# Kernel optimization log

Measured on AMD Instinct MI355X. Metric: run time of the kernel, lower is better.

## Reference

```python
import jax, jax.numpy as jnp
import numpy as np

EMB = 64
HEADS = 8
POOL = 2          # instruction_pool_size
TOK = 10          # tokens_per_instruction
CAP = 32          # max_capped_distances per axis -> tables have 2*CAP-1 rows


def setup_inputs() -> dict:
    key = jax.random.key(0)
    ks = jax.random.split(key, 8)
    scale = float(np.sqrt(6.0 / (TOK + EMB)))  # xavier-ish; exact init irrelevant for math
    return {
        "enc_cross": jax.random.uniform(ks[0], (POOL, TOK, EMB), jnp.float32, -scale, scale),
        "enc_h": jax.random.uniform(ks[1], (2 * CAP - 1, EMB), jnp.float32, -scale, scale),
        "enc_w": jax.random.uniform(ks[2], (2 * CAP - 1, EMB), jnp.float32, -scale, scale),
        "enc_d": jax.random.uniform(ks[3], (2 * CAP - 1, EMB), jnp.float32, -scale, scale),
        "w_cross": jax.random.uniform(ks[4], (HEADS, EMB), jnp.float32, -scale, scale),
        "w_h": jax.random.uniform(ks[5], (HEADS, EMB), jnp.float32, -scale, scale),
        "w_w": jax.random.uniform(ks[6], (HEADS, EMB), jnp.float32, -scale, scale),
        "w_d": jax.random.uniform(ks[7], (HEADS, EMB), jnp.float32, -scale, scale),
        "dim_q": 4116,
        "dim_k": 4116,
        "dim_i": 20,
        "dim_h": 16,
        "dim_w": 16,
        "dim_d": 16,
    }


def _rel_embed(n, table):
    # table: [2*cap-1, emb]; returns gathered relative-position embeddings [n, n, emb]
    cap = (table.shape[0] + 1) // 2
    r = jnp.arange(n)
    idx = jnp.clip(r[None, :] - r[:, None] + cap - 1, 0, 2 * cap - 2)
    return table[idx]


def reference(enc_cross, enc_h, enc_w, enc_d, w_cross, w_h, w_w, w_d,
              dim_q, dim_k, dim_i, dim_h, dim_w, dim_d):
    tok = enc_cross.shape[1]
    emb = enc_cross.shape[-1]
    heads = w_cross.shape[0]
    inv_temperature = emb ** -0.5

    # instruction -> content embeddings: first n_cat tables concatenated (label_indices=None path)
    n_cat = dim_i // tok
    cross_emb = enc_cross[:n_cat].reshape(1, n_cat * tok, emb)  # [1, dim_i, emb]

    row_e = _rel_embed(dim_h, enc_h)  # [h, h, emb]
    col_e = _rel_embed(dim_w, enc_w)  # [w, w, emb]
    dep_e = _rel_embed(dim_d, enc_d)  # [d, d, emb]

    cross_s = jnp.einsum('hc,bnc->bhn', w_cross, cross_emb)        # [1, heads, dim_i]
    row_s = jnp.einsum('hc,nmc->hnm', w_h, row_e)[None]            # [1, heads, h, h]
    col_s = jnp.einsum('hc,nmc->hnm', w_w, col_e)[None]            # [1, heads, w, w]
    dep_s = jnp.einsum('hc,nmc->hnm', w_d, dep_e)[None]            # [1, heads, d, d]

    # broadcast-add over (i j k | l m n) -> [1, heads, h, w, d, h, w, d]
    content = (row_s[:, :, :, None, None, :, None, None]
               + col_s[:, :, None, :, None, None, :, None]
               + dep_s[:, :, None, None, :, None, None, :]) / 3.0
    S = dim_h * dim_w * dim_d
    content = content.reshape(1, heads, S, S)

    scores = jnp.zeros((1, heads, dim_q, dim_k), jnp.float32)
    # instruction bias block: rows dim_i:, cols :dim_i
    scores = scores.at[:, :, dim_i:, :dim_i].set(
        jnp.broadcast_to(cross_s[:, :, None, :], (1, heads, dim_q - dim_i, dim_i)))
    # content bias block: rows dim_i:, cols dim_i:
    scores = scores.at[:, :, dim_i:, dim_i:].set(content)
    return scores * inv_temperature
```

## Files before the change

kernel.cpp:

```cpp
#include <hip/hip_runtime.h>


#define EMB 64
#define NHEADS 8
#define DIM_I 20
#define DIM_Q 4116
#define NCHUNK 1029

__global__ __launch_bounds__(256) void tables_kernel(
    const float* __restrict__ enc_cross,
    const float* __restrict__ enc_h,
    const float* __restrict__ enc_w,
    const float* __restrict__ enc_d,
    const float* __restrict__ w_cross,
    const float* __restrict__ w_h,
    const float* __restrict__ w_w,
    const float* __restrict__ w_d,
    float* __restrict__ tabs)
{
    const int tid = blockIdx.x * blockDim.x + threadIdx.x;
    const int total = NHEADS * DIM_I + 3 * NHEADS * 256;
    if (tid >= total) return;

    if (tid < NHEADS * DIM_I) {
        const int h = tid / DIM_I;
        const int n = tid % DIM_I;
        const float* wv = w_cross + h * EMB;
        const float* ev = enc_cross + n * EMB;
        float acc = 0.f;
        #pragma unroll
        for (int c = 0; c < EMB; ++c) acc += wv[c] * ev[c];
        tabs[tid] = acc * 0.125f;
    } else {
        const int u = tid - NHEADS * DIM_I;
        const int table = u >> 11;
        const int v = u & 2047;
        const int h = v >> 8;
        const int i = (v >> 4) & 15;
        const int l = v & 15;
        const int ridx = l - i + 31;
        const float* wv;
        const float* ev;
        if (table == 0)      { wv = w_h + h * EMB; ev = enc_h + ridx * EMB; }
        else if (table == 1) { wv = w_w + h * EMB; ev = enc_w + ridx * EMB; }
        else                 { wv = w_d + h * EMB; ev = enc_d + ridx * EMB; }
        float acc = 0.f;
        #pragma unroll
        for (int c = 0; c < EMB; ++c) acc += wv[c] * ev[c];
        tabs[tid] = acc * (0.125f / 3.0f);
    }
}

__global__ __launch_bounds__(256) void fill_kernel(
    const float* __restrict__ tabs, float* __restrict__ out)
{
    const int q = blockIdx.x;
    const int h = blockIdx.y;

    float4* rowp = (float4*)(out + ((size_t)h * DIM_Q + q) * DIM_Q);

    if (q < DIM_I) {
        const float4 z = make_float4(0.f, 0.f, 0.f, 0.f);
        for (int t = threadIdx.x; t < NCHUNK; t += 256) rowp[t] = z;
        return;
    }

    const float* cross  = tabs + h * DIM_I;
    const float* row_s  = tabs + 160 + h * 256;
    const float* col_s  = tabs + 160 + 2048 + h * 256;
    const float* dep_s  = tabs + 160 + 4096 + h * 256;

    const int r  = q - DIM_I;
    const int i  = r >> 8;
    const int j  = (r >> 4) & 15;
    const int kk = r & 15;
    const float* rs_row = row_s + i * 16;
    const float* cs_row = col_s + j * 16;
    const float* ds_row = dep_s + kk * 16;

    for (int t = threadIdx.x; t < NCHUNK; t += 256) {
        float4 v;
        if (t < 5) {
            const int k0 = 4 * t;
            v.x = cross[k0 + 0];
            v.y = cross[k0 + 1];
            v.z = cross[k0 + 2];
            v.w = cross[k0 + 3];
        } else {
            const int c0 = 4 * t - DIM_I;
            const int l  = c0 >> 8;
            const int m  = (c0 >> 4) & 15;
            const int n0 = c0 & 15;
            const float base = rs_row[l] + cs_row[m];
            v.x = base + ds_row[n0 + 0];
            v.y = base + ds_row[n0 + 1];
            v.z = base + ds_row[n0 + 2];
            v.w = base + ds_row[n0 + 3];
        }
        rowp[t] = v;
    }
}

extern "C" void kernel_launch(void* const* d_in, const int* in_sizes, int n_in,
                              void* d_out, int out_size, void* d_ws, size_t ws_size,
                              hipStream_t stream)
{
    const float* enc_cross = (const float*)d_in[0];
    const float* enc_h     = (const float*)d_in[1];
    const float* enc_w     = (const float*)d_in[2];
    const float* enc_d     = (const float*)d_in[3];
    const float* w_cross   = (const float*)d_in[4];
    const float* w_h       = (const float*)d_in[5];
    const float* w_w       = (const float*)d_in[6];
    const float* w_d       = (const float*)d_in[7];

    float* tabs = (float*)d_ws;

    tables_kernel<<<dim3(25), dim3(256), 0, stream>>>(
        enc_cross, enc_h, enc_w, enc_d, w_cross, w_h, w_w, w_d, tabs);

    fill_kernel<<<dim3(DIM_Q, NHEADS), dim3(256), 0, stream>>>(
        tabs, (float*)d_out);
}
```

Baseline: 567.1 us.

## Restructure fill with LDS-staged tables, nontemporal stores, wave-parallel table dots

The table kernel now computes each 64-element dot product with one wave and a shuffle reduction, which launches far more threads. The fill kernel now has each block write 16 consecutive rows for a fixed (i,j) pair. It stages the row+col base sums and the depth table in LDS and writes with nontemporal vector stores. The 20 zero rows are split across two dedicated blocks per head. The aim is to cut per-element global table reads and cache pollution in this write-bound ~540 MB output, at the cost of fewer, larger blocks (2064 total) and a serial kk loop per block.

New measurement: 611.1 us. 1.08x slower.

```diff
diff --git a/kernel.cpp b/kernel.cpp
--- a/kernel.cpp
+++ b/kernel.cpp
@@ -6,6 +6,12 @@
 #define DIM_I 20
 #define DIM_Q 4116
 #define NCHUNK 1029
+#define OFF_ROW 160
+#define OFF_COL (160 + 2048)
+#define OFF_DEP (160 + 4096)
+#define N_DOTS 6304
+
+typedef float v4f __attribute__((ext_vector_type(4)));
 
 __global__ __launch_bounds__(256) void tables_kernel(
     const float* __restrict__ enc_cross,
@@ -18,86 +24,91 @@
     const float* __restrict__ w_d,
     float* __restrict__ tabs)
 {
-    const int tid = blockIdx.x * blockDim.x + threadIdx.x;
-    const int total = NHEADS * DIM_I + 3 * NHEADS * 256;
-    if (tid >= total) return;
+    const int wid  = (blockIdx.x * 256 + threadIdx.x) >> 6;
+    const int lane = threadIdx.x & 63;
+    if (wid >= N_DOTS) return;
 
-    if (tid < NHEADS * DIM_I) {
-        const int h = tid / DIM_I;
-        const int n = tid % DIM_I;
-        const float* wv = w_cross + h * EMB;
-        const float* ev = enc_cross + n * EMB;
-        float acc = 0.f;
-        #pragma unroll
-        for (int c = 0; c < EMB; ++c) acc += wv[c] * ev[c];
-        tabs[tid] = acc * 0.125f;
+    const float* wv;
+    const float* ev;
+    float scale;
+    int outidx;
+    if (wid < 160) {
+        const int h = wid / DIM_I;
+        const int n = wid % DIM_I;
+        wv = w_cross + h * EMB;
+        ev = enc_cross + n * EMB;
+        scale = 0.125f;
+        outidx = wid;
     } else {
-        const int u = tid - NHEADS * DIM_I;
+        const int u = wid - 160;
         const int table = u >> 11;
         const int v = u & 2047;
         const int h = v >> 8;
         const int i = (v >> 4) & 15;
         const int l = v & 15;
         const int ridx = l - i + 31;
-        const float* wv;
-        const float* ev;
         if (table == 0)      { wv = w_h + h * EMB; ev = enc_h + ridx * EMB; }
         else if (table == 1) { wv = w_w + h * EMB; ev = enc_w + ridx * EMB; }
         else                 { wv = w_d + h * EMB; ev = enc_d + ridx * EMB; }
-        float acc = 0.f;
-        #pragma unroll
-        for (int c = 0; c < EMB; ++c) acc += wv[c] * ev[c];
-        tabs[tid] = acc * (0.125f / 3.0f);
+        scale = 0.125f / 3.0f;
+        outidx = 160 + u;
     }
+
+    float p = wv[lane] * ev[lane];
+    #pragma unroll
+    for (int off = 32; off >= 1; off >>= 1)
+        p += __shfl_xor(p, off, 64);
+    if (lane == 0) tabs[outidx] = p * scale;
 }
 
 __global__ __launch_bounds__(256) void fill_kernel(
     const float* __restrict__ tabs, float* __restrict__ out)
 {
-    const int q = blockIdx.x;
-    const int h = blockIdx.y;
+    const int h   = blockIdx.y;
+    const int r   = blockIdx.x;
+    const int tid = threadIdx.x;
+    float* outh = out + (size_t)h * DIM_Q * DIM_Q;
 
-    float4* rowp = (float4*)(out + ((size_t)h * DIM_Q + q) * DIM_Q);
-
-    if (q < DIM_I) {
-        const float4 z = make_float4(0.f, 0.f, 0.f, 0.f);
-        for (int t = threadIdx.x; t < NCHUNK; t += 256) rowp[t] = z;
+    if (r >= 256) {
+        v4f* p = (v4f*)outh + (size_t)(r - 256) * 10290;
+        const v4f z = {0.f, 0.f, 0.f, 0.f};
+        for (int t = tid; t < 10290; t += 256)
+            __builtin_nontemporal_store(z, p + t);
         return;
     }
 
-    const float* cross  = tabs + h * DIM_I;
-    const float* row_s  = tabs + 160 + h * 256;
-    const float* col_s  = tabs + 160 + 2048 + h * 256;
-    const float* dep_s  = tabs + 160 + 4096 + h * 256;
+    __shared__ __align__(16) float Base[256];
+    __shared__ __align__(16) float dep[256];
+    __shared__ float cross20[DIM_I];
 
-    const int r  = q - DIM_I;
-    const int i  = r >> 8;
-    const int j  = (r >> 4) & 15;
-    const int kk = r & 15;
-    const float* rs_row = row_s + i * 16;
-    const float* cs_row = col_s + j * 16;
-    const float* ds_row = dep_s + kk * 16;
+    const int i = r >> 4;
+    const int j = r & 15;
+    Base[tid] = tabs[OFF_ROW + h * 256 + i * 16 + (tid >> 4)]
+              + tabs[OFF_COL + h * 256 + j * 16 + (tid & 15)];
+    dep[tid] = tabs[OFF_DEP + h * 256 + tid];
+    if (tid < DIM_I) cross20[tid] = tabs[h * DIM_I + tid];
+    __syncthreads();
 
-    for (int t = threadIdx.x; t < NCHUNK; t += 256) {
-        float4 v;
-        if (t < 5) {
-            const int k0 = 4 * t;
-            v.x = cross[k0 + 0];
-            v.y = cross[k0 + 1];
-            v.z = cross[k0 + 2];
-            v.w = cross[k0 + 3];
-        } else {
-            const int c0 = 4 * t - DIM_I;
-            const int l  = c0 >> 8;
-            const int m  = (c0 >> 4) & 15;
-            const int n0 = c0 & 15;
-            const float base = rs_row[l] + cs_row[m];
-            v.x = base + ds_row[n0 + 0];
-            v.y = base + ds_row[n0 + 1];
-            v.z = base + ds_row[n0 + 2];
-            v.w = base + ds_row[n0 + 3];
+    const int q0 = DIM_I + i * 256 + j * 16;
+    for (int kk = 0; kk < 16; ++kk) {
+        v4f* rowp = (v4f*)(outh + (size_t)(q0 + kk) * DIM_Q);
+        const float* ds = dep + kk * 16;
+        for (int t = tid; t < NCHUNK; t += 256) {
+            v4f v;
+            if (t < 5) {
+                const int k0 = 4 * t;
+                v.x = cross20[k0 + 0];
+                v.y = cross20[k0 + 1];
+                v.z = cross20[k0 + 2];
+                v.w = cross20[k0 + 3];
+            } else {
+                const int c0 = 4 * t - DIM_I;
+                const float b = Base[c0 >> 4];
+                const v4f d = *(const v4f*)(ds + (c0 & 15));
+                v = d + b;
+            }
+            __builtin_nontemporal_store(v, rowp + t);
         }
-        rowp[t] = v;
     }
 }
 
@@ -116,9 +127,9 @@
 
     float* tabs = (float*)d_ws;
 
-    tables_kernel<<<dim3(25), dim3(256), 0, stream>>>(
+    tables_kernel<<<dim3((N_DOTS * 64 + 255) / 256), dim3(256), 0, stream>>>(
         enc_cross, enc_h, enc_w, enc_d, w_cross, w_h, w_w, w_d, tabs);
 
-    fill_kernel<<<dim3(DIM_Q, NHEADS), dim3(256), 0, stream>>>(
+    fill_kernel<<<dim3(258, NHEADS), dim3(256), 0, stream>>>(
         tabs, (float*)d_out);
 }
```
